# Performance work log

Measured on AMD Instinct MI355X. Metric: run time of the kernel, lower is better.

The kernel has to match this reference:

```python
import jax, jax.numpy as jnp
import numpy as np

B, D, C = 8192, 256, 128
MARGIN = 0.5
REPULSION_WEIGHT = 1.0
ALPHA = 0.5
BETA = 0.5
EPS = 1e-6  # F.pairwise_distance default eps, added to the difference vector


def make_centers(num_classes=C, embedding_dim=D):
    # center[k] is +/-1 one-hot along axis (k % embedding_dim)
    idx = np.arange(num_classes)
    centers = np.zeros((num_classes, embedding_dim), dtype=np.float32)
    centers[idx, idx % embedding_dim] = np.where(idx % 2 == 0, 1.0, -1.0)
    return jnp.asarray(centers)


def setup_inputs() -> dict:
    key = jax.random.key(0)
    k1, k2, k3 = jax.random.split(key, 3)
    features = jax.random.normal(k1, (B, D), dtype=jnp.float32)
    classification = jax.random.normal(k2, (B, C), dtype=jnp.float32)
    labels = jax.random.randint(k3, (B,), 0, C, dtype=jnp.int32)
    return {"features": features, "classification": classification, "labels": labels}


def _sculpted_loss(embeddings, labels, centers):
    b = embeddings.shape[0]
    # attractive: MSE to per-sample class center, mean over all elements
    center_targets = centers[labels]  # [B, D]
    attractive = jnp.mean((embeddings - center_targets) ** 2)

    # repulsive: for pairs i<j with different labels,
    # relu(margin - ||e_i - e_j + eps||_2)^2, summed then / (B(B-1)/2).
    sq_norm = jnp.sum(embeddings ** 2, axis=1)          # [B]
    row_sum = jnp.sum(embeddings, axis=1)               # [B]
    gram = embeddings @ embeddings.T                    # [B, B]
    sq = (sq_norm[:, None] + sq_norm[None, :] - 2.0 * gram
          + 2.0 * EPS * (row_sum[:, None] - row_sum[None, :])
          + embeddings.shape[1] * (EPS * EPS))
    dist = jnp.sqrt(jnp.maximum(sq, 1e-12))             # [B, B]

    iu = jnp.triu(jnp.ones((b, b), dtype=bool), k=1)    # i < j
    diff_label = labels[:, None] != labels[None, :]
    mask = iu & diff_label
    hinge = jnp.maximum(MARGIN - dist, 0.0)
    repulsive = jnp.sum(jnp.where(mask, hinge * hinge, 0.0))
    repulsive = repulsive / (b * (b - 1) / 2.0)

    return attractive + REPULSION_WEIGHT * repulsive


def reference(features, classification, labels):
    centers = make_centers()
    # cross entropy (mean over batch)
    logp = jax.nn.log_softmax(classification, axis=-1)
    ce = -jnp.mean(jnp.take_along_axis(logp, labels[:, None].astype(jnp.int32), axis=1)[:, 0])
    contrastive = _sculpted_loss(features, labels, centers)
    return BETA * contrastive + ALPHA * ce
```

## Files before the change

### kernel.cpp

```cpp
#include <hip/hip_runtime.h>
#include <stdint.h>

#define B_N   8192
#define D_DIM 256
#define C_CLS 128
#define EPSV  1e-6f
#define DEPS  (256.0f * EPSV * EPSV)
#define NT    64
#define NTRI  (NT * (NT + 1) / 2)

typedef __bf16 bf16x8 __attribute__((ext_vector_type(8)));
typedef float  f32x4  __attribute__((ext_vector_type(4)));

__device__ __forceinline__ unsigned short f2bf(float v) {
    unsigned u = __float_as_uint(v);
    u += 0x7fff + ((u >> 16) & 1);
    return (unsigned short)(u >> 16);
}


__global__ __launch_bounds__(256) void k_rowstats(
        const float* __restrict__ feat, const int* __restrict__ labels,
        unsigned short* __restrict__ ebf, float* __restrict__ aR,
        float* __restrict__ bC, float* __restrict__ attrP) {
    int t = threadIdx.x, lane = t & 63, w = t >> 6;
    int row = blockIdx.x * 4 + w;
    const float4* src = (const float4*)(feat + (size_t)row * D_DIM);
    float4 f = src[lane];
    ushort4 p;
    p.x = f2bf(f.x); p.y = f2bf(f.y); p.z = f2bf(f.z); p.w = f2bf(f.w);
    ((ushort4*)(ebf + (size_t)row * D_DIM))[lane] = p;

    int lab = labels[row];
    float sq = f.x*f.x + f.y*f.y + f.z*f.z + f.w*f.w;
    float sm = f.x + f.y + f.z + f.w;
    float arr[4] = {f.x, f.y, f.z, f.w};
    float pick = ((lab >> 2) == lane) ? arr[lab & 3] : 0.f;
    #pragma unroll
    for (int off = 32; off; off >>= 1) {
        sq   += __shfl_xor(sq, off);
        sm   += __shfl_xor(sm, off);
        pick += __shfl_xor(pick, off);
    }
    __shared__ float wsum[4];
    if (lane == 0) {
        aR[row] = sq + 2.f * EPSV * sm;
        bC[row] = sq - 2.f * EPSV * sm + DEPS;
        float s = (lab & 1) ? -1.f : 1.f;
        wsum[w] = sq - 2.f * s * pick + 1.f;
    }
    __syncthreads();
    if (t == 0) attrP[blockIdx.x] = wsum[0] + wsum[1] + wsum[2] + wsum[3];
}

__global__ __launch_bounds__(256) void k_ce(
        const float* __restrict__ cls, const int* __restrict__ labels,
        float* __restrict__ ceP) {
    int t = threadIdx.x, lane = t & 63, w = t >> 6;
    int row = blockIdx.x * 4 + w;
    const float2* src = (const float2*)(cls + (size_t)row * C_CLS);
    float2 f = src[lane];
    float mx = fmaxf(f.x, f.y);
    #pragma unroll
    for (int off = 32; off; off >>= 1) mx = fmaxf(mx, __shfl_xor(mx, off));
    float es = expf(f.x - mx) + expf(f.y - mx);
    int lab = labels[row];
    float pick = ((lab >> 1) == lane) ? ((lab & 1) ? f.y : f.x) : 0.f;
    #pragma unroll
    for (int off = 32; off; off >>= 1) {
        es   += __shfl_xor(es, off);
        pick += __shfl_xor(pick, off);
    }
    __shared__ float wsum[4];
    if (lane == 0) wsum[w] = -(pick - mx - logf(es));
    __syncthreads();
    if (t == 0) ceP[blockIdx.x] = wsum[0] + wsum[1] + wsum[2] + wsum[3];
}

__global__ __launch_bounds__(256) void k_gram(
        const unsigned short* __restrict__ ebf, const float* __restrict__ aR,
        const float* __restrict__ bC, const int* __restrict__ labels,
        float* __restrict__ repP) {
    __shared__ __align__(16) unsigned short As[128 * 64];
    __shared__ __align__(16) unsigned short Bs[128 * 64];
    __shared__ float aM[128], bN[128];
    __shared__ int   lM[128], lN[128];
    __shared__ float wred[4];

    int t = threadIdx.x, lane = t & 63, w = t >> 6;

    int bid = blockIdx.x, tm = 0;
    while (bid >= NT - tm) { bid -= NT - tm; tm++; }
    int tn = tm + bid;

    if (t < 128) {
        int i = tm * 128 + t;
        aM[t] = aR[i]; lM[t] = labels[i];
    } else {
        int j = tn * 128 + (t - 128);
        bN[t - 128] = bC[j]; lN[t - 128] = labels[j];
    }

    f32x4 acc[4][4] = {};
    int wr = w >> 1, wc = w & 1;
    int rowA = t >> 3;
    int klog = ((t & 7) ^ (rowA & 7)) * 8;
    int quad = lane >> 4, l15 = lane & 15;
    int sw   = (l15 & 7);

    for (int k0 = 0; k0 < D_DIM; k0 += 64) {
        #pragma unroll
        for (int r = 0; r < 4; r++) {
            const unsigned short* ga = ebf + (size_t)(tm * 128 + r * 32 + rowA) * D_DIM + k0 + klog;
            const unsigned short* gb = ebf + (size_t)(tn * 128 + r * 32 + rowA) * D_DIM + k0 + klog;
            unsigned short* la = As + (r * 256 + w * 64) * 8;
            unsigned short* lb = Bs + (r * 256 + w * 64) * 8;
            __builtin_amdgcn_global_load_lds((const __attribute__((address_space(1))) void*)ga,
                                             (__attribute__((address_space(3))) void*)la, 16, 0, 0);
            __builtin_amdgcn_global_load_lds((const __attribute__((address_space(1))) void*)gb,
                                             (__attribute__((address_space(3))) void*)lb, 16, 0, 0);
        }
        __syncthreads();

        int m0 = wr * 64, n0 = wc * 64;
        #pragma unroll
        for (int kk = 0; kk < 64; kk += 32) {
            int kg   = quad | (kk >> 3);
            int xofs = ((kg ^ sw) << 3);
            bf16x8 av[4], bv[4];
            #pragma unroll
            for (int mi = 0; mi < 4; mi++)
                av[mi] = *(const bf16x8*)(As + (m0 + mi * 16 + l15) * 64 + xofs);
            #pragma unroll
            for (int ni = 0; ni < 4; ni++)
                bv[ni] = *(const bf16x8*)(Bs + (n0 + ni * 16 + l15) * 64 + xofs);
            #pragma unroll
            for (int mi = 0; mi < 4; mi++)
                #pragma unroll
                for (int ni = 0; ni < 4; ni++)
                    acc[mi][ni] = __builtin_amdgcn_mfma_f32_16x16x32_bf16(av[mi], bv[ni], acc[mi][ni], 0, 0, 0);
        }
        __syncthreads();
    }

    float am[16], bn[4];
    #pragma unroll
    for (int ni = 0; ni < 4; ni++) bn[ni] = bN[wc * 64 + ni * 16 + l15];
    #pragma unroll
    for (int mi = 0; mi < 4; mi++)
        #pragma unroll
        for (int r = 0; r < 4; r++)
            am[mi * 4 + r] = aM[wr * 64 + mi * 16 + quad * 4 + r];

    float minv = 1e30f;
    #pragma unroll
    for (int mi = 0; mi < 4; mi++)
        #pragma unroll
        for (int ni = 0; ni < 4; ni++)
            #pragma unroll
            for (int r = 0; r < 4; r++)
                minv = fminf(minv, fmaf(-2.f, acc[mi][ni][r], am[mi * 4 + r] + bn[ni]));
    #pragma unroll
    for (int off = 32; off; off >>= 1) minv = fminf(minv, __shfl_xor(minv, off));

    float rep = 0.f;
    if (minv < 0.25f) {
        #pragma unroll
        for (int mi = 0; mi < 4; mi++) {
            #pragma unroll
            for (int ni = 0; ni < 4; ni++) {
                int n  = wc * 64 + ni * 16 + l15;
                int jg = tn * 128 + n;
                #pragma unroll
                for (int r = 0; r < 4; r++) {
                    int m  = wr * 64 + mi * 16 + quad * 4 + r;
                    int ig = tm * 128 + m;
                    float sq   = fmaf(-2.f, acc[mi][ni][r], am[mi * 4 + r] + bn[ni]);
                    float dist = sqrtf(fmaxf(sq, 1e-12f));
                    float h    = fmaxf(0.5f - dist, 0.f);
                    rep += (lM[m] != lN[n] && ig < jg) ? h * h : 0.f;
                }
            }
        }
        #pragma unroll
        for (int off = 32; off; off >>= 1) rep += __shfl_xor(rep, off);
    }
    if (lane == 0) wred[w] = rep;
    __syncthreads();
    if (t == 0) repP[blockIdx.x] = wred[0] + wred[1] + wred[2] + wred[3];
}

__global__ __launch_bounds__(256) void k_final(
        const float* __restrict__ P, float* __restrict__ out) {
    int t = threadIdx.x, lane = t & 63, w = t >> 6;
    float a = 0.f, c = 0.f, r = 0.f;
    for (int i = t; i < 2048; i += 256) { a += P[i]; c += P[2048 + i]; }
    for (int i = t; i < NTRI; i += 256) r += P[4096 + i];
    #pragma unroll
    for (int off = 32; off; off >>= 1) {
        a += __shfl_xor(a, off);
        c += __shfl_xor(c, off);
        r += __shfl_xor(r, off);
    }
    __shared__ float sa[4], sc[4], sr[4];
    if (lane == 0) { sa[w] = a; sc[w] = c; sr[w] = r; }
    __syncthreads();
    if (t == 0) {
        float attr = (sa[0] + sa[1] + sa[2] + sa[3]) / (float)((size_t)B_N * D_DIM);
        float ce   = (sc[0] + sc[1] + sc[2] + sc[3]) / (float)B_N;
        float rep  = (sr[0] + sr[1] + sr[2] + sr[3]) / ((float)B_N * (float)(B_N - 1) * 0.5f);
        out[0] = 0.5f * (attr + rep) + 0.5f * ce;
    }
}

extern "C" void kernel_launch(void* const* d_in, const int* in_sizes, int n_in,
                              void* d_out, int out_size, void* d_ws, size_t ws_size,
                              hipStream_t stream) {
    const float* feat   = (const float*)d_in[0];
    const float* cls    = (const float*)d_in[1];
    const int*   labels = (const int*)d_in[2];
    float* out = (float*)d_out;

    float*          P    = (float*)d_ws;
    unsigned short* ebf  = (unsigned short*)((char*)d_ws + 32768);
    float*          aR   = (float*)((char*)d_ws + 32768 + (size_t)B_N * D_DIM * 2);
    float*          bC   = aR + B_N;
    float*          attrP = P;
    float*          ceP   = P + 2048;
    float*          repP  = P + 4096;

    k_rowstats<<<2048, 256, 0, stream>>>(feat, labels, ebf, aR, bC, attrP);
    k_ce      <<<2048, 256, 0, stream>>>(cls, labels, ceP);
    k_gram    <<<NTRI, 256, 0, stream>>>(ebf, aR, bC, labels, repP);
    k_final   <<<1, 256, 0, stream>>>(P, out);
}
```

Before: 104.6 us.

## Fuse row-stats and cross-entropy kernels; widen gram K-tile to 128

Merges the feature row-statistics kernel and the cross-entropy kernel into one prep kernel, removing a launch and sharing the label load and shuffle reductions. The gram kernel now stages 128-wide K slices, so it runs two outer iterations instead of four and half as many barrier pairs. The LDS swizzle is reworked to XOR over 16 chunks to match the wider rows. LDS use doubles to 64KB per block, which may reduce occupancy.

```diff
diff --git a/kernel.cpp b/kernel.cpp
--- a/kernel.cpp
+++ b/kernel.cpp
@@ -19,70 +19,63 @@
 }
 
 
-__global__ __launch_bounds__(256) void k_rowstats(
-        const float* __restrict__ feat, const int* __restrict__ labels,
-        unsigned short* __restrict__ ebf, float* __restrict__ aR,
-        float* __restrict__ bC, float* __restrict__ attrP) {
+__global__ __launch_bounds__(256) void k_prep(
+        const float* __restrict__ feat, const float* __restrict__ cls,
+        const int* __restrict__ labels, unsigned short* __restrict__ ebf,
+        float* __restrict__ aR, float* __restrict__ bC,
+        float* __restrict__ attrP, float* __restrict__ ceP) {
     int t = threadIdx.x, lane = t & 63, w = t >> 6;
     int row = blockIdx.x * 4 + w;
+    int lab = labels[row];
+
     const float4* src = (const float4*)(feat + (size_t)row * D_DIM);
     float4 f = src[lane];
     ushort4 p;
     p.x = f2bf(f.x); p.y = f2bf(f.y); p.z = f2bf(f.z); p.w = f2bf(f.w);
     ((ushort4*)(ebf + (size_t)row * D_DIM))[lane] = p;
 
-    int lab = labels[row];
     float sq = f.x*f.x + f.y*f.y + f.z*f.z + f.w*f.w;
     float sm = f.x + f.y + f.z + f.w;
     float arr[4] = {f.x, f.y, f.z, f.w};
     float pick = ((lab >> 2) == lane) ? arr[lab & 3] : 0.f;
+
+    const float2* csrc = (const float2*)(cls + (size_t)row * C_CLS);
+    float2 c2 = csrc[lane];
+    float mx = fmaxf(c2.x, c2.y);
+    #pragma unroll
+    for (int off = 32; off; off >>= 1) mx = fmaxf(mx, __shfl_xor(mx, off));
+    float es = expf(c2.x - mx) + expf(c2.y - mx);
+    float cpick = ((lab >> 1) == lane) ? ((lab & 1) ? c2.y : c2.x) : 0.f;
+
     #pragma unroll
     for (int off = 32; off; off >>= 1) {
-        sq   += __shfl_xor(sq, off);
-        sm   += __shfl_xor(sm, off);
-        pick += __shfl_xor(pick, off);
-    }
-    __shared__ float wsum[4];
+        sq    += __shfl_xor(sq, off);
+        sm    += __shfl_xor(sm, off);
+        pick  += __shfl_xor(pick, off);
+        es    += __shfl_xor(es, off);
+        cpick += __shfl_xor(cpick, off);
+    }
+    __shared__ float wsumA[4], wsumC[4];
     if (lane == 0) {
         aR[row] = sq + 2.f * EPSV * sm;
         bC[row] = sq - 2.f * EPSV * sm + DEPS;
         float s = (lab & 1) ? -1.f : 1.f;
-        wsum[w] = sq - 2.f * s * pick + 1.f;
+        wsumA[w] = sq - 2.f * s * pick + 1.f;
+        wsumC[w] = -(cpick - mx - logf(es));
     }
     __syncthreads();
-    if (t == 0) attrP[blockIdx.x] = wsum[0] + wsum[1] + wsum[2] + wsum[3];
-}
-
-__global__ __launch_bounds__(256) void k_ce(
-        const float* __restrict__ cls, const int* __restrict__ labels,
-        float* __restrict__ ceP) {
-    int t = threadIdx.x, lane = t & 63, w = t >> 6;
-    int row = blockIdx.x * 4 + w;
-    const float2* src = (const float2*)(cls + (size_t)row * C_CLS);
-    float2 f = src[lane];
-    float mx = fmaxf(f.x, f.y);
-    #pragma unroll
-    for (int off = 32; off; off >>= 1) mx = fmaxf(mx, __shfl_xor(mx, off));
-    float es = expf(f.x - mx) + expf(f.y - mx);
-    int lab = labels[row];
-    float pick = ((lab >> 1) == lane) ? ((lab & 1) ? f.y : f.x) : 0.f;
-    #pragma unroll
-    for (int off = 32; off; off >>= 1) {
-        es   += __shfl_xor(es, off);
-        pick += __shfl_xor(pick, off);
-    }
-    __shared__ float wsum[4];
-    if (lane == 0) wsum[w] = -(pick - mx - logf(es));
-    __syncthreads();
-    if (t == 0) ceP[blockIdx.x] = wsum[0] + wsum[1] + wsum[2] + wsum[3];
+    if (t == 0) {
+        attrP[blockIdx.x] = wsumA[0] + wsumA[1] + wsumA[2] + wsumA[3];
+        ceP[blockIdx.x]   = wsumC[0] + wsumC[1] + wsumC[2] + wsumC[3];
+    }
 }
 
 __global__ __launch_bounds__(256) void k_gram(
         const unsigned short* __restrict__ ebf, const float* __restrict__ aR,
         const float* __restrict__ bC, const int* __restrict__ labels,
         float* __restrict__ repP) {
-    __shared__ __align__(16) unsigned short As[128 * 64];
-    __shared__ __align__(16) unsigned short Bs[128 * 64];
+    __shared__ __align__(16) unsigned short As[128 * 128];
+    __shared__ __align__(16) unsigned short Bs[128 * 128];
     __shared__ float aM[128], bN[128];
     __shared__ int   lM[128], lN[128];
     __shared__ float wred[4];
@@ -103,18 +96,18 @@
 
     f32x4 acc[4][4] = {};
     int wr = w >> 1, wc = w & 1;
-    int rowA = t >> 3;
-    int klog = ((t & 7) ^ (rowA & 7)) * 8;
+    int srow = t >> 4;
+    int scol = ((t & 15) ^ srow) * 8;
     int quad = lane >> 4, l15 = lane & 15;
-    int sw   = (l15 & 7);
-
-    for (int k0 = 0; k0 < D_DIM; k0 += 64) {
-        #pragma unroll
-        for (int r = 0; r < 4; r++) {
-            const unsigned short* ga = ebf + (size_t)(tm * 128 + r * 32 + rowA) * D_DIM + k0 + klog;
-            const unsigned short* gb = ebf + (size_t)(tn * 128 + r * 32 + rowA) * D_DIM + k0 + klog;
-            unsigned short* la = As + (r * 256 + w * 64) * 8;
-            unsigned short* lb = Bs + (r * 256 + w * 64) * 8;
+
+    for (int k0 = 0; k0 < D_DIM; k0 += 128) {
+        #pragma unroll
+        for (int i = 0; i < 8; i++) {
+            int row = i * 16 + srow;
+            const unsigned short* ga = ebf + (size_t)(tm * 128 + row) * D_DIM + k0 + scol;
+            const unsigned short* gb = ebf + (size_t)(tn * 128 + row) * D_DIM + k0 + scol;
+            unsigned short* la = As + i * 2048 + (w * 64) * 8;
+            unsigned short* lb = Bs + i * 2048 + (w * 64) * 8;
             __builtin_amdgcn_global_load_lds((const __attribute__((address_space(1))) void*)ga,
                                              (__attribute__((address_space(3))) void*)la, 16, 0, 0);
             __builtin_amdgcn_global_load_lds((const __attribute__((address_space(1))) void*)gb,
@@ -124,16 +117,19 @@
 
         int m0 = wr * 64, n0 = wc * 64;
         #pragma unroll
-        for (int kk = 0; kk < 64; kk += 32) {
-            int kg   = quad | (kk >> 3);
-            int xofs = ((kg ^ sw) << 3);
+        for (int kk = 0; kk < 128; kk += 32) {
+            int kc = (kk >> 3) | quad;
             bf16x8 av[4], bv[4];
             #pragma unroll
-            for (int mi = 0; mi < 4; mi++)
-                av[mi] = *(const bf16x8*)(As + (m0 + mi * 16 + l15) * 64 + xofs);
-            #pragma unroll
-            for (int ni = 0; ni < 4; ni++)
-                bv[ni] = *(const bf16x8*)(Bs + (n0 + ni * 16 + l15) * 64 + xofs);
+            for (int mi = 0; mi < 4; mi++) {
+                int r = m0 + mi * 16 + l15;
+                av[mi] = *(const bf16x8*)(As + r * 128 + ((kc ^ l15) << 3));
+            }
+            #pragma unroll
+            for (int ni = 0; ni < 4; ni++) {
+                int r = n0 + ni * 16 + l15;
+                bv[ni] = *(const bf16x8*)(Bs + r * 128 + ((kc ^ l15) << 3));
+            }
             #pragma unroll
             for (int mi = 0; mi < 4; mi++)
                 #pragma unroll
@@ -229,8 +225,7 @@
     float*          ceP   = P + 2048;
     float*          repP  = P + 4096;
 
-    k_rowstats<<<2048, 256, 0, stream>>>(feat, labels, ebf, aR, bC, attrP);
-    k_ce      <<<2048, 256, 0, stream>>>(cls, labels, ceP);
-    k_gram    <<<NTRI, 256, 0, stream>>>(ebf, aR, bC, labels, repP);
-    k_final   <<<1, 256, 0, stream>>>(P, out);
-}
+    k_prep <<<2048, 256, 0, stream>>>(feat, cls, labels, ebf, aR, bC, attrP, ceP);
+    k_gram <<<NTRI, 256, 0, stream>>>(ebf, aR, bC, labels, repP);
+    k_final<<<1, 256, 0, stream>>>(P, out);
+}
```

Result: faster. 100.9 us (-3.5%).
